# Kernel optimization log

Measured on AMD Instinct MI355X. Metric: run time of the kernel, lower is better.

Reference implementation:

```python
import jax, jax.numpy as jnp
import numpy as np

B_SZ, L, H, D, N, R, K = 2, 1024, 2048, 4096, 16, 128, 4


def setup_inputs() -> dict:
    key = jax.random.key(0)
    ks = jax.random.split(key, 10)
    s = lambda *sh: 1.0 / np.sqrt(sh[-1])
    inp = {
        "hidden_states": jax.random.normal(ks[0], (B_SZ, L, H), jnp.float32),
        "in_proj_w": jax.random.normal(ks[1], (2 * D, H), jnp.float32) * s(H),
        "conv_w": jax.random.normal(ks[2], (D, 1, K), jnp.float32) * s(K),
        "conv_b": jax.random.normal(ks[3], (D,), jnp.float32) * 0.02,
        "x_proj_w": jax.random.normal(ks[4], (R + 2 * N, D), jnp.float32) * s(D),
        "dt_proj_w": jax.random.normal(ks[5], (D, R), jnp.float32) * s(R),
        "dt_proj_b": jax.random.normal(ks[6], (D,), jnp.float32) * 0.02,
        # A_log = log(arange(1, N+1)) broadcast over D, as in the module init
        "A_log": jnp.broadcast_to(jnp.log(jnp.arange(1, N + 1, dtype=jnp.float32))[None, :], (D, N)),
        "D_param": jnp.ones((D,), jnp.float32),
        "out_proj_w": jax.random.normal(ks[7], (H, D), jnp.float32) * s(D),
    }
    return inp


def _mamba_forward(hidden_states, in_proj_w, conv_w, conv_b, x_proj_w,
                   dt_proj_w, dt_proj_b, A_log, D_param, out_proj_w):
    silu = jax.nn.silu
    # in_proj: [B,L,H] @ [H,2D] -> [B,L,2D] -> [B,2D,L]
    proj = jnp.einsum("blh,ph->bpl", hidden_states, in_proj_w)
    u, gate = jnp.split(proj, 2, axis=1)  # each [B,D,L]
    # depthwise causal conv1d (padding K-1 on the left, then first L outputs)
    u = jax.lax.conv_general_dilated(
        u, conv_w, window_strides=(1,), padding=[(K - 1, 0)],
        dimension_numbers=("NCH", "OIH", "NCH"), feature_group_count=D,
    ) + conv_b[None, :, None]
    u = silu(u)  # [B,D,L]
    # x_proj on [B,L,D]
    ssm_params = jnp.einsum("bdl,pd->blp", u, x_proj_w)  # [B,L,R+2N]
    time_step, Bmat, Cmat = jnp.split(ssm_params, [R, R + N], axis=-1)
    # dt_proj + softplus -> [B,D,L]
    dt = jnp.einsum("blr,dr->bld", time_step, dt_proj_w) + dt_proj_b
    dt = jax.nn.softplus(dt).transpose(0, 2, 1)  # [B,D,L]
    A = -jnp.exp(A_log)  # [D,N]

    # selective scan over time; carry ssm_state [B,D,N]
    def step(state, xs):
        dt_t, B_t, C_t, u_t = xs  # [B,D],[B,N],[B,N],[B,D]
        dA = jnp.exp(A[None] * dt_t[:, :, None])          # [B,D,N]
        dBu = dt_t[:, :, None] * B_t[:, None, :] * u_t[:, :, None]
        state = dA * state + dBu
        y_t = jnp.einsum("bdn,bn->bd", state, C_t)        # [B,D]
        return state, y_t

    xs = (dt.transpose(2, 0, 1),          # [L,B,D]
          Bmat.transpose(1, 0, 2),        # [L,B,N]
          Cmat.transpose(1, 0, 2),        # [L,B,N]
          u.transpose(2, 0, 1))           # [L,B,D]
    init = jnp.zeros((hidden_states.shape[0], D, N), hidden_states.dtype)
    _, ys = jax.lax.scan(step, init, xs)   # ys [L,B,D]
    y = ys.transpose(1, 2, 0)              # [B,D,L]
    y = y + u * D_param[None, :, None]
    y = y * silu(gate)
    # out_proj: [B,L,D] @ [D,H]
    return jnp.einsum("bdl,hd->blh", y, out_proj_w)


def reference(hidden_states, in_proj_w, conv_w, conv_b, x_proj_w,
              dt_proj_w, dt_proj_b, A_log, D_param, out_proj_w):
    return _mamba_forward(hidden_states, in_proj_w, conv_w, conv_b, x_proj_w,
                          dt_proj_w, dt_proj_b, A_log, D_param, out_proj_w)
```

## Files before the change

### kernel.cpp

```cpp
#include <hip/hip_runtime.h>

#define L_SEQ 1024
#define DD 4096
#define NC 32
#define CT 32

typedef short bf16x8 __attribute__((ext_vector_type(8)));
typedef float f32x4 __attribute__((ext_vector_type(4)));
typedef unsigned short u16;

typedef const __attribute__((address_space(1))) void gas_t;
typedef __attribute__((address_space(3))) void las_t;

__device__ inline u16 f2bf(float f) {
  unsigned int u = __float_as_uint(f);
  u = (u + 0x7FFFu + ((u >> 16) & 1u)) >> 16;
  return (u16)u;
}

__device__ inline float bf2f(u16 v) {
  return __uint_as_float(((unsigned int)v) << 16);
}

__device__ inline float softplusf(float x) {
  return x > 20.f ? x : log1pf(expf(x));
}

__global__ __launch_bounds__(256) void cast_all_k(
    const float* __restrict__ hs, const float* __restrict__ w_in,
    const float* __restrict__ xw, const float* __restrict__ dtw,
    const float* __restrict__ ow, u16* __restrict__ hs_bf,
    u16* __restrict__ win_bf, u16* __restrict__ xw_bf,
    u16* __restrict__ dtw_bf, u16* __restrict__ ow_bf) {
  const int blk = blockIdx.x;
  const float* s;
  u16* d;
  int base;
  if (blk < 4096)        { s = hs;   d = hs_bf;  base = blk; }
  else if (blk < 20480)  { s = w_in; d = win_bf; base = blk - 4096; }
  else if (blk < 21120)  { s = xw;   d = xw_bf;  base = blk - 20480; }
  else if (blk < 21632)  { s = dtw;  d = dtw_bf; base = blk - 21120; }
  else                   { s = ow;   d = ow_bf;  base = blk - 21632; }
  const int i = (base * 256 + threadIdx.x) * 4;
  float4 v = *(const float4*)(s + i);
  ushort4 o;
  o.x = f2bf(v.x); o.y = f2bf(v.y); o.z = f2bf(v.z); o.w = f2bf(v.w);
  *(ushort4*)(d + i) = o;
}

__global__ __launch_bounds__(256) void reduce4b_k(const u16* __restrict__ p,
                                                  float* __restrict__ out,
                                                  long n) {
  long i = ((long)blockIdx.x * 256 + threadIdx.x) * 8;
  if (i >= n) return;
  uint4 a = *(const uint4*)(p + i);
  uint4 b = *(const uint4*)(p + n + i);
  uint4 c = *(const uint4*)(p + 2 * n + i);
  uint4 d = *(const uint4*)(p + 3 * n + i);
  const u16* qa = (const u16*)&a;
  const u16* qb = (const u16*)&b;
  const u16* qc = (const u16*)&c;
  const u16* qd = (const u16*)&d;
  float o[8];
#pragma unroll
  for (int j = 0; j < 8; j++)
    o[j] = (bf2f(qa[j]) + bf2f(qb[j])) + (bf2f(qc[j]) + bf2f(qd[j]));
  *(float4*)(out + i) = make_float4(o[0], o[1], o[2], o[3]);
  *(float4*)(out + i + 4) = make_float4(o[4], o[5], o[6], o[7]);
}

__global__ __launch_bounds__(256) void xproj_fin_k(const float* __restrict__ parts,
                                                   u16* __restrict__ ts,
                                                   float* __restrict__ ssm) {
  const int idx = blockIdx.x * 256 + threadIdx.x;
  float s = 0.f;
#pragma unroll
  for (int z = 0; z < 16; z++) s += parts[z * 327680 + idx];
  const int row = idx / 160;
  const int col = idx - row * 160;
  if (col < 128) ts[row * 128 + col] = f2bf(s);
  else ssm[idx] = s;
}

template <int CMODE, bool SWZ>
__global__ __launch_bounds__(512, 2) void gemm256(const u16* __restrict__ A,
                                                  const u16* __restrict__ B,
                                                  void* __restrict__ Cv,
                                                  int Nld, int K, int kc,
                                                  long zstride) {
  __shared__ u16 lds[3][2][8192];
  const int tid = threadIdx.x;
  const int lane = tid & 63, wid = tid >> 6;
  const int wm = wid >> 2, wn = wid & 3;
  int ty = blockIdx.y, tx = blockIdx.x;
  if (SWZ) {
    int flat = blockIdx.y * 32 + blockIdx.x;
    int xcd = flat & 7, pos = flat >> 3;
    ty = (xcd & 1) * 4 + (pos >> 3);
    tx = (xcd >> 1) * 8 + (pos & 7);
  }
  const long tm = (long)ty * 256, tn = (long)tx * 256;

  const long ks0 = (CMODE == 2) ? (long)blockIdx.z * kc : 0;

  const int srow = tid >> 2;
  const int sks = (((tid & 3) ^ ((srow >> 1) & 3))) * 8;
  const u16* gA0 = A + (tm + srow) * (long)K + ks0 + sks;
  const u16* gA1 = A + (tm + 128 + srow) * (long)K + ks0 + sks;
  const u16* gB0 = B + (tn + srow) * (long)K + ks0 + sks;
  const u16* gB1 = B + (tn + 128 + srow) * (long)K + ks0 + sks;
  const int sb0 = wid * 512;
  const int sb1 = 4096 + wid * 512;

  f32x4 acc[8][4] = {};

  const int lr = lane & 15, kq = lane >> 4;
  const int arow = wm * 128 + lr;
  const int brow = wn * 64 + lr;
  const int granA = (kq ^ ((arow >> 1) & 3)) * 8;
  const int granB = (kq ^ ((brow >> 1) & 3)) * 8;

  const int KT = kc >> 5;

#define STG(buf, kt)                                                           \
  {                                                                            \
    const long ko_ = (long)(kt) << 5;                                          \
    __builtin_amdgcn_global_load_lds((gas_t*)(gA0 + ko_),                      \
                                     (las_t*)&lds[buf][0][sb0], 16, 0, 0);     \
    __builtin_amdgcn_global_load_lds((gas_t*)(gA1 + ko_),                      \
                                     (las_t*)&lds[buf][0][sb1], 16, 0, 0);     \
    __builtin_amdgcn_global_load_lds((gas_t*)(gB0 + ko_),                      \
                                     (las_t*)&lds[buf][1][sb0], 16, 0, 0);     \
    __builtin_amdgcn_global_load_lds((gas_t*)(gB1 + ko_),                      \
                                     (las_t*)&lds[buf][1][sb1], 16, 0, 0);     \
  }

  STG(0, 0);
  STG(1, 1);
  STG(2, 2);

  int buf = 0;
  for (int kt = 0; kt < KT; ++kt) {
    if (kt + 3 <= KT)
      asm volatile("s_waitcnt vmcnt(8)" ::: "memory");
    else if (kt + 2 == KT)
      asm volatile("s_waitcnt vmcnt(4)" ::: "memory");
    else
      asm volatile("s_waitcnt vmcnt(0)" ::: "memory");
    __builtin_amdgcn_s_barrier();

    bf16x8 af[8], bfr[4];
#pragma unroll
    for (int n = 0; n < 4; n++)
      bfr[n] = *(const bf16x8*)&lds[buf][1][(brow + n * 16) * 32 + granB];
#pragma unroll
    for (int m = 0; m < 8; m++)
      af[m] = *(const bf16x8*)&lds[buf][0][(arow + m * 16) * 32 + granA];
#pragma unroll
    for (int m = 0; m < 8; m++)
#pragma unroll
      for (int n = 0; n < 4; n++)
        acc[m][n] = __builtin_amdgcn_mfma_f32_16x16x32_bf16(af[m], bfr[n],
                                                            acc[m][n], 0, 0, 0);
    asm volatile("s_waitcnt lgkmcnt(0)" ::: "memory");
    __builtin_amdgcn_s_barrier();
    if (kt + 3 < KT) STG(buf, kt + 3);
    buf = (buf == 2) ? 0 : buf + 1;
  }
#undef STG

  const int rg = (lane >> 4) * 4;
#pragma unroll
  for (int m = 0; m < 8; m++) {
    const long gr = tm + wm * 128 + m * 16 + rg;
#pragma unroll
    for (int n = 0; n < 4; n++) {
      const long gc = tn + wn * 64 + n * 16 + lr;
#pragma unroll
      for (int r = 0; r < 4; r++) {
        if (CMODE == 1)
          ((u16*)Cv)[(gr + r) * (long)Nld + gc] = f2bf(acc[m][n][r]);
        else
          ((u16*)Cv)[(long)blockIdx.z * zstride + (gr + r) * (long)Nld + gc] =
              f2bf(acc[m][n][r]);
      }
    }
  }
}

template <bool CLAMP_N, int MODE>
__global__ __launch_bounds__(256) void gemm_bt(const u16* __restrict__ A,
                                               const u16* __restrict__ B,
                                               void* __restrict__ Cv,
                                               const float* __restrict__ ebias,
                                               int Nv, int K, int ldc, int kc,
                                               long zs) {
  __shared__ u16 lA[128 * 32];
  __shared__ u16 lB[128 * 32];
  const int tid = threadIdx.x;
  const int lane = tid & 63, wid = tid >> 6;
  const int wm = wid >> 1, wn = wid & 1;
  const long tm = (long)blockIdx.y * 128, tn = (long)blockIdx.x * 128;

  f32x4 acc[4][4] = {};

  const int roff = lane >> 2;
  const int sks = (((lane & 3) ^ ((roff >> 1) & 3))) * 8;
  const int c0 = wid * 2, c1 = c0 + 1;
  const long ra0 = tm + c0 * 16 + roff;
  const long ra1 = tm + c1 * 16 + roff;
  long rb0 = tn + c0 * 16 + roff;
  long rb1 = tn + c1 * 16 + roff;
  if (CLAMP_N) {
    if (rb0 >= Nv) rb0 = Nv - 1;
    if (rb1 >= Nv) rb1 = Nv - 1;
  }
  const u16* gA0 = A + ra0 * K + sks;
  const u16* gA1 = A + ra1 * K + sks;
  const u16* gB0 = B + rb0 * K + sks;
  const u16* gB1 = B + rb1 * K + sks;
  u16* sA0 = &lA[c0 * 512];
  u16* sA1 = &lA[c1 * 512];
  u16* sB0 = &lB[c0 * 512];
  u16* sB1 = &lB[c1 * 512];

  int ks0 = 0, ks1 = K;
  if (MODE == 2) { ks0 = blockIdx.z * kc; ks1 = ks0 + kc; }

  const int lr = lane & 15, kq = lane >> 4;
  const int arow = wm * 64 + lr, brow = wn * 64 + lr;
  const int granA = (kq ^ ((arow >> 1) & 3)) * 8;
  const int granB = (kq ^ ((brow >> 1) & 3)) * 8;

  for (int ks = ks0; ks < ks1; ks += 32) {
    __builtin_amdgcn_global_load_lds((gas_t*)(gA0 + ks), (las_t*)sA0, 16, 0, 0);
    __builtin_amdgcn_global_load_lds((gas_t*)(gA1 + ks), (las_t*)sA1, 16, 0, 0);
    __builtin_amdgcn_global_load_lds((gas_t*)(gB0 + ks), (las_t*)sB0, 16, 0, 0);
    __builtin_amdgcn_global_load_lds((gas_t*)(gB1 + ks), (las_t*)sB1, 16, 0, 0);
    __syncthreads();
    bf16x8 af[4], bfr[4];
#pragma unroll
    for (int i = 0; i < 4; i++) {
      af[i]  = *(const bf16x8*)&lA[(arow + i * 16) * 32 + granA];
      bfr[i] = *(const bf16x8*)&lB[(brow + i * 16) * 32 + granB];
    }
#pragma unroll
    for (int i = 0; i < 4; i++)
#pragma unroll
      for (int j = 0; j < 4; j++)
        acc[i][j] = __builtin_amdgcn_mfma_f32_16x16x32_bf16(af[i], bfr[j],
                                                            acc[i][j], 0, 0, 0);
    __syncthreads();
  }

  float* Cf = (MODE == 2) ? (float*)Cv + (long)blockIdx.z * zs : (float*)Cv;

  const int rg = (lane >> 4) * 4;
#pragma unroll
  for (int i = 0; i < 4; i++) {
    const long gr = tm + wm * 64 + i * 16 + rg;
#pragma unroll
    for (int j = 0; j < 4; j++) {
      const long gc = tn + wn * 64 + j * 16 + lr;
      if (CLAMP_N && gc >= Nv) continue;
      float bias = 0.f;
      if (MODE == 1) bias = ebias[gc];
#pragma unroll
      for (int r = 0; r < 4; r++) {
        float v = acc[i][j][r];
        if (MODE == 1)
          ((u16*)Cv)[(gr + r) * (long)ldc + gc] = f2bf(softplusf(v + bias));
        else
          Cf[(gr + r) * (long)ldc + gc] = v;
      }
    }
  }
}

__global__ __launch_bounds__(256) void conv_silu_k(const u16* __restrict__ projb,
                                                   const float* __restrict__ cw,
                                                   const float* __restrict__ cb,
                                                   u16* __restrict__ ub) {
  const int gid = blockIdx.x * 256 + threadIdx.x;
  const int d = (gid & 511) * 8;
  const int bl = gid >> 9;
  const int l = bl & (L_SEQ - 1);
  const u16* pp = projb + (long)bl * 8192 + d;
  const uint4 zero = make_uint4(0, 0, 0, 0);
  uint4 t0 = *(const uint4*)pp;
  uint4 t1 = (l >= 1) ? *(const uint4*)(pp - 8192) : zero;
  uint4 t2 = (l >= 2) ? *(const uint4*)(pp - 16384) : zero;
  uint4 t3 = (l >= 3) ? *(const uint4*)(pp - 24576) : zero;
  const u16* q0 = (const u16*)&t0;
  const u16* q1 = (const u16*)&t1;
  const u16* q2 = (const u16*)&t2;
  const u16* q3 = (const u16*)&t3;
  float4 b0 = *(const float4*)(cb + d);
  float4 b1 = *(const float4*)(cb + d + 4);
  const float* bb = &b0.x;
  u16 ov[8];
#pragma unroll
  for (int j = 0; j < 8; j++) {
    const float4 w = *(const float4*)(cw + (d + j) * 4);
    float s = (j < 4) ? ((const float*)&b0)[j] : ((const float*)&b1)[j - 4];
    s += w.w * bf2f(q0[j]);
    s += w.z * bf2f(q1[j]);
    s += w.y * bf2f(q2[j]);
    s += w.x * bf2f(q3[j]);
    const float r = s / (1.f + expf(-s));
    ov[j] = f2bf(r);
  }
  (void)bb;
  *(uint4*)(ub + (long)bl * DD + d) = *(uint4*)ov;
}

__global__ __launch_bounds__(256) void scan_p1(const u16* __restrict__ dt,
                                               const u16* __restrict__ u,
                                               const float* __restrict__ ssm,
                                               const float* __restrict__ A_log,
                                               float* __restrict__ Sbuf,
                                               float* __restrict__ Pbuf) {
  __shared__ float sBC[CT * 32];
  __shared__ u16 dtl[CT][256];
  __shared__ u16 ul[CT][256];
  const int tid = threadIdx.x;
  const int d0 = blockIdx.x * 256;
  const int d = d0 + tid;
  const int c = blockIdx.y, b = blockIdx.z;
  const long blbase = (long)b * L_SEQ + (long)c * CT;
  for (int i = tid; i < CT * 32; i += 256) {
    int tt = i >> 5, j = i & 31;
    sBC[i] = ssm[(blbase + tt) * 160 + 128 + j];
  }
  const u16* dtg = dt + blbase * DD + d0;
  const u16* ug  = u  + blbase * DD + d0;
#pragma unroll
  for (int it = 0; it < 4; ++it) {
    const int ck = it * 256 + tid;
    const int row = ck >> 5, ch = (ck & 31) * 8;
    *(uint4*)&dtl[row][ch] = *(const uint4*)(dtg + (long)row * DD + ch);
    *(uint4*)&ul[row][ch]  = *(const uint4*)(ug  + (long)row * DD + ch);
  }
  __syncthreads();
  float a2[16], st[16], pr[16];
#pragma unroll
  for (int g = 0; g < 4; g++) {
    float4 al = *(const float4*)(A_log + d * 16 + g * 4);
    a2[g*4+0] = -expf(al.x) * 1.4426950408889634f;
    a2[g*4+1] = -expf(al.y) * 1.4426950408889634f;
    a2[g*4+2] = -expf(al.z) * 1.4426950408889634f;
    a2[g*4+3] = -expf(al.w) * 1.4426950408889634f;
  }
#pragma unroll
  for (int n = 0; n < 16; n++) { st[n] = 0.f; pr[n] = 1.f; }
  for (int tt = 0; tt < CT; tt++) {
    const float dtv = bf2f(dtl[tt][tid]);
    const float uv = bf2f(ul[tt][tid]);
    const float dtu = dtv * uv;
    const float4* Bv = (const float4*)&sBC[tt * 32];
#pragma unroll
    for (int g = 0; g < 4; g++) {
      const float4 Bg = Bv[g];
      float e;
      e = exp2f(a2[g*4+0]*dtv); st[g*4+0] = e*st[g*4+0] + dtu*Bg.x; pr[g*4+0] *= e;
      e = exp2f(a2[g*4+1]*dtv); st[g*4+1] = e*st[g*4+1] + dtu*Bg.y; pr[g*4+1] *= e;
      e = exp2f(a2[g*4+2]*dtv); st[g*4+2] = e*st[g*4+2] + dtu*Bg.z; pr[g*4+2] *= e;
      e = exp2f(a2[g*4+3]*dtv); st[g*4+3] = e*st[g*4+3] + dtu*Bg.w; pr[g*4+3] *= e;
    }
  }
  const long base = (((long)b * NC + c) * DD + d) * 16;
#pragma unroll
  for (int g = 0; g < 4; g++) {
    *(float4*)(Sbuf + base + g * 4) = make_float4(st[g*4+0], st[g*4+1], st[g*4+2], st[g*4+3]);
    *(float4*)(Pbuf + base + g * 4) = make_float4(pr[g*4+0], pr[g*4+1], pr[g*4+2], pr[g*4+3]);
  }
}

__global__ __launch_bounds__(256) void scan_p2(const float* __restrict__ Sbuf,
                                               const float* __restrict__ Pbuf,
                                               float* __restrict__ carry) {
  const int idx = blockIdx.x * 256 + threadIdx.x;
  const int ng = idx & 3;
  const int d = (idx >> 2) & (DD - 1);
  const int b = idx >> 14;
  const long stride = (long)DD * 16;
  long base = ((long)b * NC * DD + d) * 16 + ng * 4;
  float4 P = *(const float4*)(Pbuf + base);
  float4 S = *(const float4*)(Sbuf + base);
  float4 cr = make_float4(0.f, 0.f, 0.f, 0.f);
  for (int c = 0; c < NC; c++) {
    float4 Pn, Sn;
    if (c + 1 < NC) {
      Pn = *(const float4*)(Pbuf + base + stride);
      Sn = *(const float4*)(Sbuf + base + stride);
    }
    *(float4*)(carry + base) = cr;
    cr.x = P.x * cr.x + S.x;
    cr.y = P.y * cr.y + S.y;
    cr.z = P.z * cr.z + S.z;
    cr.w = P.w * cr.w + S.w;
    P = Pn; S = Sn;
    base += stride;
  }
}

__global__ __launch_bounds__(256) void scan_p3(const u16* __restrict__ dt,
                                               const u16* __restrict__ u,
                                               const float* __restrict__ ssm,
                                               const u16* __restrict__ projb,
                                               const float* __restrict__ A_log,
                                               const float* __restrict__ Dp,
                                               const float* __restrict__ carry,
                                               u16* __restrict__ yb) {
  __shared__ float sBC[CT * 32];
  __shared__ u16 dtl[CT][256];
  __shared__ u16 ul[CT][256];
  const int tid = threadIdx.x;
  const int d0 = blockIdx.x * 256;
  const int d = d0 + tid;
  const int c = blockIdx.y, b = blockIdx.z;
  const long blbase = (long)b * L_SEQ + (long)c * CT;
  for (int i = tid; i < CT * 32; i += 256) {
    int tt = i >> 5, j = i & 31;
    sBC[i] = ssm[(blbase + tt) * 160 + 128 + j];
  }
  const u16* dtg = dt + blbase * DD + d0;
  const u16* ug  = u  + blbase * DD + d0;
#pragma unroll
  for (int it = 0; it < 4; ++it) {
    const int ck = it * 256 + tid;
    const int row = ck >> 5, ch = (ck & 31) * 8;
    *(uint4*)&dtl[row][ch] = *(const uint4*)(dtg + (long)row * DD + ch);
    *(uint4*)&ul[row][ch]  = *(const uint4*)(ug  + (long)row * DD + ch);
  }
  __syncthreads();
  float a2[16], st[16];
#pragma unroll
  for (int g = 0; g < 4; g++) {
    float4 al = *(const float4*)(A_log + d * 16 + g * 4);
    a2[g*4+0] = -expf(al.x) * 1.4426950408889634f;
    a2[g*4+1] = -expf(al.y) * 1.4426950408889634f;
    a2[g*4+2] = -expf(al.z) * 1.4426950408889634f;
    a2[g*4+3] = -expf(al.w) * 1.4426950408889634f;
  }
  const long cbase = (((long)b * NC + c) * DD + d) * 16;
#pragma unroll
  for (int g = 0; g < 4; g++) {
    float4 cv = *(const float4*)(carry + cbase + g * 4);
    st[g*4+0] = cv.x; st[g*4+1] = cv.y; st[g*4+2] = cv.z; st[g*4+3] = cv.w;
  }
  const float dp = Dp[d];
  const u16* gp = projb + blbase * 8192 + DD + d;
  u16 gnext = gp[0];
  for (int tt = 0; tt < CT; tt++) {
    const u16 gcur = gnext;
    if (tt + 1 < CT) gnext = gp[(tt + 1) * 8192];
    const float dtv = bf2f(dtl[tt][tid]);
    const float uv = bf2f(ul[tt][tid]);
    const float dtu = dtv * uv;
    float acc = 0.f;
    const float4* Bv = (const float4*)&sBC[tt * 32];
    const float4* Cv = Bv + 4;
#pragma unroll
    for (int g = 0; g < 4; g++) {
      const float4 Bg = Bv[g];
      const float4 Cg = Cv[g];
      float e;
      e = exp2f(a2[g*4+0]*dtv); st[g*4+0] = e*st[g*4+0] + dtu*Bg.x; acc += st[g*4+0]*Cg.x;
      e = exp2f(a2[g*4+1]*dtv); st[g*4+1] = e*st[g*4+1] + dtu*Bg.y; acc += st[g*4+1]*Cg.y;
      e = exp2f(a2[g*4+2]*dtv); st[g*4+2] = e*st[g*4+2] + dtu*Bg.z; acc += st[g*4+2]*Cg.z;
      e = exp2f(a2[g*4+3]*dtv); st[g*4+3] = e*st[g*4+3] + dtu*Bg.w; acc += st[g*4+3]*Cg.w;
    }
    const float g = bf2f(gcur);
    const float yv = (acc + uv * dp) * (g / (1.f + expf(-g)));
    yb[(blbase + tt) * DD + d] = f2bf(yv);
  }
}

extern "C" void kernel_launch(void* const* d_in, const int* in_sizes, int n_in,
                              void* d_out, int out_size, void* d_ws, size_t ws_size,
                              hipStream_t stream) {
  const float* hs     = (const float*)d_in[0];
  const float* w_in   = (const float*)d_in[1];
  const float* conv_w = (const float*)d_in[2];
  const float* conv_b = (const float*)d_in[3];
  const float* xw     = (const float*)d_in[4];
  const float* dtw    = (const float*)d_in[5];
  const float* dtb    = (const float*)d_in[6];
  const float* A_log  = (const float*)d_in[7];
  const float* Dp     = (const float*)d_in[8];
  const float* ow     = (const float*)d_in[9];
  float* out = (float*)d_out;

  constexpr size_t SZ_HS_BF  = 2048ull * 2048 * 2;
  constexpr size_t SZ_WIN_BF = 8192ull * 2048 * 2;
  constexpr size_t SZ_PROJ   = 2048ull * 8192 * 2;
  constexpr size_t SZ_UBF    = 2048ull * 4096 * 2;
  constexpr size_t SZ_XW_BF  = 160ull * 4096 * 2;
  constexpr size_t SZ_SSM    = 2048ull * 160 * 4;
  constexpr size_t SZ_TS_BF  = 2048ull * 128 * 2;
  constexpr size_t SZ_DTW_BF = 4096ull * 128 * 2;
  constexpr size_t SZ_DT     = 2048ull * 4096 * 2;
  constexpr size_t SZ_OW_BF  = 2048ull * 4096 * 2;
  constexpr size_t SZ_YBF    = 2048ull * 4096 * 2;
  constexpr size_t SZ_SCAN   = 2ull * NC * DD * 16 * 4;
  constexpr size_t TOTAL = SZ_HS_BF + SZ_WIN_BF + SZ_PROJ + SZ_UBF +
                           SZ_XW_BF + SZ_SSM + SZ_TS_BF + SZ_DTW_BF + SZ_DT +
                           SZ_OW_BF + SZ_YBF + 3 * SZ_SCAN;
  if (ws_size < TOTAL) return;

  char* w = (char*)d_ws;
  u16* hs_bf   = (u16*)w;   w += SZ_HS_BF;
  u16* win_bf  = (u16*)w;   w += SZ_WIN_BF;
  u16* projb   = (u16*)w;   w += SZ_PROJ;
  u16* u_bf    = (u16*)w;   w += SZ_UBF;
  u16* xw_bf   = (u16*)w;   w += SZ_XW_BF;
  float* ssm   = (float*)w; w += SZ_SSM;
  u16* ts_bf   = (u16*)w;   w += SZ_TS_BF;
  u16* dtw_bf  = (u16*)w;   w += SZ_DTW_BF;
  u16* dt_bf   = (u16*)w;   w += SZ_DT;
  u16* ow_bf   = (u16*)w;   w += SZ_OW_BF;
  u16* y_bf    = (u16*)w;   w += SZ_YBF;
  float* Sbuf  = (float*)w; w += SZ_SCAN;
  float* Pbuf  = (float*)w; w += SZ_SCAN;
  float* carry = (float*)w; w += SZ_SCAN;

  float* partsx = Sbuf;
  u16* parts = win_bf;

  cast_all_k<<<29824, 256, 0, stream>>>(hs, w_in, xw, dtw, ow,
                                        hs_bf, win_bf, xw_bf, dtw_bf, ow_bf);

  gemm256<1, true><<<dim3(32, 8), 512, 0, stream>>>(
      hs_bf, win_bf, projb, 8192, 2048, 2048, 0);

  conv_silu_k<<<4096, 256, 0, stream>>>(projb, conv_w, conv_b, u_bf);

  gemm_bt<true, 2><<<dim3(2, 16, 16), 256, 0, stream>>>(
      u_bf, xw_bf, partsx, nullptr, 160, 4096, 160, 256, 327680);

  xproj_fin_k<<<1280, 256, 0, stream>>>(partsx, ts_bf, ssm);

  gemm_bt<false, 1><<<dim3(32, 16), 256, 0, stream>>>(
      ts_bf, dtw_bf, dt_bf, dtb, 4096, 128, 4096, 0, 0);

  scan_p1<<<dim3(16, NC, 2), 256, 0, stream>>>(dt_bf, u_bf, ssm, A_log, Sbuf, Pbuf);
  scan_p2<<<128, 256, 0, stream>>>(Sbuf, Pbuf, carry);
  scan_p3<<<dim3(16, NC, 2), 256, 0, stream>>>(dt_bf, u_bf, ssm, projb, A_log, Dp,
                                               carry, y_bf);

  gemm256<2, false><<<dim3(8, 8, 4), 512, 0, stream>>>(
      y_bf, ow_bf, parts, 2048, 4096, 1024, 2048ll * 2048);
  reduce4b_k<<<2048, 256, 0, stream>>>(parts, out, 2048ll * 2048);
}
```

Baseline: 356.0 us.

## Interleave GEMM global-to-LDS prefetch with MFMA sub-steps and raise MFMA priority

Reworks the bf16 GEMM main loop so prefetch depth drops from three stages in flight to two. Each of the four global_load_lds issues for tile kt+2 is spread across four sub-phases of the MFMA work. Each sub-phase loads two A fragments, issues one staging load, runs eight MFMAs at raised s_setprio, then hits a barrier. The aim is to overlap memory issue with matrix math and cut the single large barrier stall. The cost is four barriers per k-step instead of two and less latency hiding from the shallower prefetch. It also removes an unused variable in the conv kernel.

Result: no change. 358.6 us (+0.7%).

```diff
diff --git a/kernel.cpp b/kernel.cpp
--- a/kernel.cpp
+++ b/kernel.cpp
@@ -122,52 +122,63 @@
 
   const int KT = kc >> 5;
 
-#define STG(buf, kt)                                                           \
+#define STG1(b, k, c)                                                          \
   {                                                                            \
-    const long ko_ = (long)(kt) << 5;                                          \
-    __builtin_amdgcn_global_load_lds((gas_t*)(gA0 + ko_),                      \
-                                     (las_t*)&lds[buf][0][sb0], 16, 0, 0);     \
-    __builtin_amdgcn_global_load_lds((gas_t*)(gA1 + ko_),                      \
-                                     (las_t*)&lds[buf][0][sb1], 16, 0, 0);     \
-    __builtin_amdgcn_global_load_lds((gas_t*)(gB0 + ko_),                      \
-                                     (las_t*)&lds[buf][1][sb0], 16, 0, 0);     \
-    __builtin_amdgcn_global_load_lds((gas_t*)(gB1 + ko_),                      \
-                                     (las_t*)&lds[buf][1][sb1], 16, 0, 0);     \
-  }
-
-  STG(0, 0);
-  STG(1, 1);
-  STG(2, 2);
+    const long ko_ = (long)(k) << 5;                                           \
+    if ((c) == 0)                                                              \
+      __builtin_amdgcn_global_load_lds((gas_t*)(gA0 + ko_),                    \
+                                       (las_t*)&lds[b][0][sb0], 16, 0, 0);     \
+    else if ((c) == 1)                                                         \
+      __builtin_amdgcn_global_load_lds((gas_t*)(gA1 + ko_),                    \
+                                       (las_t*)&lds[b][0][sb1], 16, 0, 0);     \
+    else if ((c) == 2)                                                         \
+      __builtin_amdgcn_global_load_lds((gas_t*)(gB0 + ko_),                    \
+                                       (las_t*)&lds[b][1][sb0], 16, 0, 0);     \
+    else                                                                       \
+      __builtin_amdgcn_global_load_lds((gas_t*)(gB1 + ko_),                    \
+                                       (las_t*)&lds[b][1][sb1], 16, 0, 0);     \
+  }
+
+  STG1(0, 0, 0); STG1(0, 0, 1); STG1(0, 0, 2); STG1(0, 0, 3);
+  if (KT > 1) { STG1(1, 1, 0); STG1(1, 1, 1); STG1(1, 1, 2); STG1(1, 1, 3); }
 
   int buf = 0;
   for (int kt = 0; kt < KT; ++kt) {
-    if (kt + 3 <= KT)
-      asm volatile("s_waitcnt vmcnt(8)" ::: "memory");
-    else if (kt + 2 == KT)
+    if (kt + 1 < KT)
       asm volatile("s_waitcnt vmcnt(4)" ::: "memory");
     else
       asm volatile("s_waitcnt vmcnt(0)" ::: "memory");
     __builtin_amdgcn_s_barrier();
 
-    bf16x8 af[8], bfr[4];
-#pragma unroll
-    for (int n = 0; n < 4; n++)
-      bfr[n] = *(const bf16x8*)&lds[buf][1][(brow + n * 16) * 32 + granB];
-#pragma unroll
-    for (int m = 0; m < 8; m++)
-      af[m] = *(const bf16x8*)&lds[buf][0][(arow + m * 16) * 32 + granA];
-#pragma unroll
-    for (int m = 0; m < 8; m++)
+    const int nb = (buf == 0) ? 2 : buf - 1;
+    const bool doS = (kt + 2) < KT;
+    bf16x8 bfr[4];
+#pragma unroll
+    for (int p = 0; p < 4; ++p) {
+      bf16x8 a0 = *(const bf16x8*)&lds[buf][0][(arow + (2 * p) * 16) * 32 + granA];
+      bf16x8 a1 = *(const bf16x8*)&lds[buf][0][(arow + (2 * p + 1) * 16) * 32 + granA];
+      if (p == 0) {
+#pragma unroll
+        for (int n = 0; n < 4; n++)
+          bfr[n] = *(const bf16x8*)&lds[buf][1][(brow + n * 16) * 32 + granB];
+      }
+      if (doS) STG1(nb, kt + 2, p);
+      asm volatile("s_waitcnt lgkmcnt(0)" ::: "memory");
+      __builtin_amdgcn_s_setprio(1);
 #pragma unroll
       for (int n = 0; n < 4; n++)
-        acc[m][n] = __builtin_amdgcn_mfma_f32_16x16x32_bf16(af[m], bfr[n],
-                                                            acc[m][n], 0, 0, 0);
-    asm volatile("s_waitcnt lgkmcnt(0)" ::: "memory");
-    __builtin_amdgcn_s_barrier();
-    if (kt + 3 < KT) STG(buf, kt + 3);
+        acc[2 * p][n] = __builtin_amdgcn_mfma_f32_16x16x32_bf16(
+            a0, bfr[n], acc[2 * p][n], 0, 0, 0);
+#pragma unroll
+      for (int n = 0; n < 4; n++)
+        acc[2 * p + 1][n] = __builtin_amdgcn_mfma_f32_16x16x32_bf16(
+            a1, bfr[n], acc[2 * p + 1][n], 0, 0, 0);
+      __builtin_amdgcn_s_setprio(0);
+      __builtin_amdgcn_s_barrier();
+    }
     buf = (buf == 2) ? 0 : buf + 1;
   }
-#undef STG
+#undef STG1
 
   const int rg = (lane >> 4) * 4;
 #pragma unroll
@@ -297,7 +308,6 @@
   const u16* q3 = (const u16*)&t3;
   float4 b0 = *(const float4*)(cb + d);
   float4 b1 = *(const float4*)(cb + d + 4);
-  const float* bb = &b0.x;
   u16 ov[8];
 #pragma unroll
   for (int j = 0; j < 8; j++) {
@@ -310,7 +320,6 @@
     const float r = s / (1.f + expf(-s));
     ov[j] = f2bf(r);
   }
-  (void)bb;
   *(uint4*)(ub + (long)bl * DD + d) = *(uint4*)ov;
 }
 
```
